# Optimization experiments

Measured on AMD Instinct MI355X. Metric: run time of the kernel, lower is better.

The kernel has to match this reference:

```python
import jax, jax.numpy as jnp
import numpy as np

G = 2048            # number of graphs in batch
NPG = 128           # nodes per graph (fixed, implied by Linear(128*hid, 1))
IN_C = 151
HID = 64
N = G * NPG
E = 2_097_152       # intra-graph edges, avg degree 8
NEG_SLOPE = 0.2


def setup_inputs() -> dict:
    key = jax.random.key(0)
    ks = jax.random.split(key, 8)
    x = jax.random.normal(ks[0], (N, IN_C), dtype=jnp.float32)
    # intra-graph random edges: pick a graph, then src/dst within it
    g = jax.random.randint(ks[1], (E,), 0, G)
    src = g * NPG + jax.random.randint(ks[2], (E,), 0, NPG)
    dst = g * NPG + jax.random.randint(ks[3], (E,), 0, NPG)
    edge_index = jnp.stack([src, dst]).astype(jnp.int32)   # [2, E]
    W1 = jax.random.normal(ks[4], (IN_C, HID), jnp.float32) / np.sqrt(IN_C)
    att_src = jax.random.normal(ks[5], (HID,), jnp.float32) * 0.1
    att_dst = jax.random.normal(ks[6], (HID,), jnp.float32) * 0.1
    b1 = jnp.zeros((HID,), jnp.float32)
    Wlin = jax.random.normal(ks[7], (NPG * HID, 1), jnp.float32) / np.sqrt(NPG * HID)
    blin = jnp.zeros((1,), jnp.float32)
    return {"x": x, "edge_index": edge_index, "W1": W1, "att_src": att_src,
            "att_dst": att_dst, "b1": b1, "Wlin": Wlin, "blin": blin}


def gat_conv(x, edge_index, W, a_src, a_dst, b):
    """PyG GATConv, heads=1, concat=True, add_self_loops=True."""
    n = x.shape[0]
    h = x @ W                                   # [N, HID] transformed features
    loops = jnp.arange(n, dtype=edge_index.dtype)
    src = jnp.concatenate([edge_index[0], loops])
    dst = jnp.concatenate([edge_index[1], loops])
    # edge score: a_src . h[j] + a_dst . h[i], j->i
    alpha = (h @ a_src)[src] + (h @ a_dst)[dst]            # [E+N]
    alpha = jax.nn.leaky_relu(alpha, NEG_SLOPE)
    # segment softmax over incoming edges of each target node
    amax = jax.ops.segment_max(alpha, dst, num_segments=n)
    ex = jnp.exp(alpha - amax[dst])
    denom = jax.ops.segment_sum(ex, dst, num_segments=n)
    w = ex / denom[dst]                                    # [E+N]
    out = jax.ops.segment_sum(h[src] * w[:, None], dst, num_segments=n)
    return out + b


def reference(x, edge_index, W1, att_src, att_dst, b1, Wlin, blin):
    h = jax.nn.relu(gat_conv(x, edge_index, W1, att_src, att_dst, b1))  # [N, HID]
    h = h.reshape(G, NPG * HID)        # linearize(x, batch): 128 nodes/graph
    logits = h @ Wlin + blin           # [G, 1]
    return jax.nn.sigmoid(logits)
```

## Files before the change

kernel.cpp:

```cpp
#include <hip/hip_runtime.h>
#include <hip/hip_bf16.h>

#define G_ 2048
#define NPG_ 128
#define INC_ 151
#define HID_ 64
#define NNODES_ (G_ * NPG_)
#define NEDGES_ 2097152

typedef __hip_bfloat16 bf16;
typedef short bf16x8v __attribute__((ext_vector_type(8)));
typedef float f32x4 __attribute__((ext_vector_type(4)));

static __device__ __forceinline__ short f2bs(float f) {
    __hip_bfloat16 b = __float2bfloat16(f);
    return __builtin_bit_cast(short, b);
}
static __device__ __forceinline__ float b2f(short s) {
    unsigned int u = ((unsigned int)(unsigned short)s) << 16;
    return __builtin_bit_cast(float, u);
}

__global__ void __launch_bounds__(256) k0_prep(const float* __restrict__ W1,
                                              bf16* __restrict__ Bt) {
    int i = blockIdx.x * 256 + threadIdx.x;
    if (i >= 64 * 168) return;
    int n = i / 168, k = i - n * 168;
    float v = (k < 151) ? W1[k * 64 + n] : 0.f;
    Bt[i] = __float2bfloat16(v);
}

__global__ void __launch_bounds__(256) k1_mfma(
        const float* __restrict__ x, const bf16* __restrict__ Bt,
        const float* __restrict__ att_src, const float* __restrict__ att_dst,
        bf16* __restrict__ h, float* __restrict__ as_, float* __restrict__ ad_) {
    __shared__ __align__(16) bf16 Bs[64 * 168];
    const int tid = threadIdx.x;
    const int rowbase = blockIdx.x * 64;

    {
        const uint4* s = (const uint4*)Bt;
        uint4* d = (uint4*)Bs;
        for (int i = tid; i < 1344; i += 256) d[i] = s[i];
    }
    __syncthreads();

    const int wv = tid >> 6, lane = tid & 63;
    const int quad = lane >> 4, m = lane & 15;
    const int row = rowbase + wv * 16 + m;
    const float* xr = x + (size_t)row * 151;

    f32x4 acc[4];
#pragma unroll
    for (int t = 0; t < 4; t++) acc[t] = (f32x4){0.f, 0.f, 0.f, 0.f};

#pragma unroll
    for (int ks = 0; ks < 5; ks++) {
        const int k0 = ks * 32 + quad * 8;
        float a[8];
        if (ks < 4) {
#pragma unroll
            for (int e = 0; e < 8; e++) a[e] = xr[k0 + e];
        } else {
#pragma unroll
            for (int e = 0; e < 8; e++) {
                int c = k0 + e;
                a[e] = (c < 151) ? xr[c] : 0.f;
            }
        }
        bf16x8v af = {f2bs(a[0]), f2bs(a[1]), f2bs(a[2]), f2bs(a[3]),
                      f2bs(a[4]), f2bs(a[5]), f2bs(a[6]), f2bs(a[7])};
#pragma unroll
        for (int t = 0; t < 4; t++) {
            bf16x8v bfr = *(const bf16x8v*)&Bs[(t * 16 + m) * 168 + k0];
            acc[t] = __builtin_amdgcn_mfma_f32_16x16x32_bf16(af, bfr, acc[t], 0, 0, 0);
        }
    }

    float as4[4], ad4[4];
#pragma unroll
    for (int t = 0; t < 4; t++) {
        as4[t] = att_src[t * 16 + m];
        ad4[t] = att_dst[t * 16 + m];
    }
#pragma unroll
    for (int r = 0; r < 4; r++) {
        float s = acc[0][r] * as4[0] + acc[1][r] * as4[1] +
                  acc[2][r] * as4[2] + acc[3][r] * as4[3];
        float d = acc[0][r] * ad4[0] + acc[1][r] * ad4[1] +
                  acc[2][r] * ad4[2] + acc[3][r] * ad4[3];
#pragma unroll
        for (int off = 1; off <= 8; off <<= 1) {
            s += __shfl_xor(s, off);
            d += __shfl_xor(d, off);
        }
        const int node = rowbase + wv * 16 + quad * 4 + r;
        if (m == 0) { as_[node] = s; ad_[node] = d; }
#pragma unroll
        for (int t = 0; t < 4; t++) {
            float val = acc[t][r];
            float oth = __shfl_xor(val, 1);
            if (!(lane & 1)) {
                unsigned short lo = (unsigned short)f2bs(val);
                unsigned short hi = (unsigned short)f2bs(oth);
                unsigned int u = ((unsigned int)hi << 16) | lo;
                *(unsigned int*)&h[(size_t)node * 64 + t * 16 + m] = u;
            }
        }
    }
}

__global__ void __launch_bounds__(256) kC1_hist(const int* __restrict__ ei,
                                                unsigned int* __restrict__ bccount) {
    __shared__ unsigned int hist[256];
    const int tid = threadIdx.x;
    hist[tid] = 0;
    __syncthreads();
    const int e0 = blockIdx.x * 8192;
    for (int e = e0 + tid; e < e0 + 8192; e += 256)
        atomicAdd(&hist[ei[e] >> 10], 1u);
    __syncthreads();
    bccount[blockIdx.x * 256 + tid] = hist[tid];
}

__global__ void __launch_bounds__(256) kC2_scan(unsigned int* __restrict__ bccount,
                                                unsigned int* __restrict__ cbase,
                                                unsigned int* __restrict__ base) {
    __shared__ unsigned int ssum[256];
    const int tid = threadIdx.x;
    unsigned int run = 0;
#pragma unroll 4
    for (int b = 0; b < 256; b++) {
        unsigned int* p = &bccount[b * 256 + tid];
        unsigned int c = *p;
        *p = run;
        run += c;
    }
    ssum[tid] = run;
    __syncthreads();
    unsigned int tot = run;
    for (int off = 1; off < 256; off <<= 1) {
        unsigned int t = (tid >= off) ? ssum[tid - off] : 0;
        __syncthreads();
        ssum[tid] += t;
        __syncthreads();
    }
    cbase[tid] = ssum[tid] - tot;
    if (tid == 255) {
        cbase[256] = ssum[255];
        base[G_] = NEDGES_;
    }
}

__global__ void __launch_bounds__(256) kC3_scatter(const int* __restrict__ ei,
                                                   const unsigned int* __restrict__ bccount,
                                                   const unsigned int* __restrict__ cbase,
                                                   unsigned int* __restrict__ rbuf) {
    __shared__ unsigned int cur[256];
    const int tid = threadIdx.x;
    cur[tid] = cbase[tid] + bccount[blockIdx.x * 256 + tid];
    __syncthreads();
    const int e0 = blockIdx.x * 8192;
    for (int e = e0 + tid; e < e0 + 8192; e += 256) {
        int s = ei[e];
        int d = ei[NEDGES_ + e];
        int bk = s >> 10;
        unsigned int pos = atomicAdd(&cur[bk], 1u);
        rbuf[pos] = (((unsigned int)s & 1023u) << 7) | ((unsigned int)d & 127u);
    }
}

__global__ void __launch_bounds__(256) kC4_fine(const unsigned int* __restrict__ rbuf,
                                                const unsigned int* __restrict__ cbase,
                                                unsigned int* __restrict__ base,
                                                unsigned short* __restrict__ eb) {
    __shared__ unsigned int lcnt[8];
    __shared__ unsigned int cur[8];
    const int tid = threadIdx.x;
    const int b = blockIdx.x;
    const unsigned int s0 = cbase[b], s1 = cbase[b + 1];
    if (tid < 8) lcnt[tid] = 0;
    __syncthreads();
    for (unsigned int i = s0 + tid; i < s1; i += 256)
        atomicAdd(&lcnt[(rbuf[i] >> 14) & 7], 1u);
    __syncthreads();
    if (tid == 0) {
        unsigned int r = 0;
#pragma unroll
        for (int j = 0; j < 8; j++) {
            base[b * 8 + j] = s0 + r;
            cur[j] = s0 + r;
            r += lcnt[j];
        }
    }
    __syncthreads();
    const int lane = tid & 63;
    for (unsigned int i = s0 + tid; i < s1; i += 256) {
        unsigned int rec = rbuf[i];
        int gl = (rec >> 14) & 7;
        unsigned long long act = __ballot(1);
        unsigned long long b0 = __ballot(gl & 1);
        unsigned long long b1 = __ballot(gl & 2);
        unsigned long long b2 = __ballot(gl & 4);
        unsigned long long m = ((gl & 1) ? b0 : ~b0) &
                               ((gl & 2) ? b1 : ~b1) &
                               ((gl & 4) ? b2 : ~b2) & act;
        int leader = __builtin_ctzll(m);
        int rank = __builtin_popcountll(m & ((1ull << lane) - 1ull));
        unsigned int bp = 0;
        if (lane == leader)
            bp = atomicAdd(&cur[gl], (unsigned int)__builtin_popcountll(m));
        bp = __shfl((int)bp, leader);
        eb[bp + rank] = (unsigned short)(rec & 0x3FFFu);
    }
}

__global__ void __launch_bounds__(256) k3_graph(
        const unsigned short* __restrict__ eb, const unsigned int* __restrict__ base,
        const bf16* __restrict__ h,
        const float* __restrict__ as_, const float* __restrict__ ad_,
        const float* __restrict__ b1, const float* __restrict__ Wlin,
        const float* __restrict__ blin, float* __restrict__ out) {
    __shared__ __align__(16) unsigned char lds[52736];
    short* Ab = (short*)lds;
    float* S = (float*)(lds + 34816);
    short* hT = (short*)(lds + 34816);
    unsigned short* ec = (unsigned short*)(lds + 30720);
    float* dinv = (float*)(lds + 52224);

    const int tid = threadIdx.x;
    const int g = blockIdx.x;
    const unsigned int gb = base[g], ge = base[g + 1];
    const float* asg = as_ + (g << 7);
    const float* adg = ad_ + (g << 7);
    const unsigned int* hgu = (const unsigned int*)(h + ((size_t)g << 13));

    const unsigned int cnt = ge - gb;
    const unsigned int ccnt = cnt > 2048u ? 2048u : cnt;
    for (unsigned int k = tid; k < ccnt; k += 256) ec[k] = eb[gb + k];
    __syncthreads();

#pragma unroll 1
    for (int p = 0; p < 4; p++) {
        for (int i = tid; i < 1024; i += 256)
            ((float4*)S)[i] = make_float4(0.f, 0.f, 0.f, 0.f);
        __syncthreads();
        if (tid < 32) {
            int node = 32 * p + tid;
            float a = asg[node] + adg[node];
            a = (a > 0.f) ? a : 0.2f * a;
            atomicAdd(&S[(tid << 7) + node], __expf(a));
        }
        for (unsigned int k = tid; k < ccnt; k += 256) {
            unsigned int v = ec[k];
            int sl = v >> 7, dl = v & 127;
            if ((dl >> 5) == p) {
                float a = asg[sl] + adg[dl];
                a = (a > 0.f) ? a : 0.2f * a;
                atomicAdd(&S[((dl & 31) << 7) + sl], __expf(a));
            }
        }
        for (unsigned int k = gb + ccnt + tid; k < ge; k += 256) {
            unsigned int v = eb[k];
            int sl = v >> 7, dl = v & 127;
            if ((dl >> 5) == p) {
                float a = asg[sl] + adg[dl];
                a = (a > 0.f) ? a : 0.2f * a;
                atomicAdd(&S[((dl & 31) << 7) + sl], __expf(a));
            }
        }
        __syncthreads();
        {
            const float4* rp = (const float4*)&S[((tid >> 3) << 7) + ((tid & 7) << 4)];
            float s = 0.f;
#pragma unroll
            for (int q = 0; q < 4; q++) {
                float4 v = rp[q];
                s += v.x + v.y + v.z + v.w;
            }
            s += __shfl_xor(s, 1);
            s += __shfl_xor(s, 2);
            s += __shfl_xor(s, 4);
            if ((tid & 7) == 0) dinv[32 * p + (tid >> 3)] = 1.f / s;
        }
        for (int c = tid; c < 512; c += 256) {
            int r = c >> 4;
            int col = (c & 15) << 3;
            float4 v0 = ((const float4*)S)[c * 2];
            float4 v1 = ((const float4*)S)[c * 2 + 1];
            bf16x8v pk = {f2bs(v0.x), f2bs(v0.y), f2bs(v0.z), f2bs(v0.w),
                          f2bs(v1.x), f2bs(v1.y), f2bs(v1.z), f2bs(v1.w)};
            *(bf16x8v*)&Ab[(32 * p + r) * 136 + col] = pk;
        }
        __syncthreads();
    }

    for (int idx = tid; idx < 4096; idx += 256) {
        unsigned int u = hgu[idx];
        int j = idx >> 5, f2 = idx & 31;
        hT[(2 * f2) * 136 + j] = (short)(u & 0xFFFF);
        hT[(2 * f2 + 1) * 136 + j] = (short)(u >> 16);
    }
    __syncthreads();

    const int w = tid >> 6, lane = tid & 63;
    const int quad = lane >> 4, m = lane & 15;
    const int i0 = w * 32;
    f32x4 acc[2][4];
#pragma unroll
    for (int mt = 0; mt < 2; mt++)
#pragma unroll
        for (int nt = 0; nt < 4; nt++) acc[mt][nt] = (f32x4){0.f, 0.f, 0.f, 0.f};

#pragma unroll
    for (int ks = 0; ks < 4; ks++) {
        const int k0 = ks * 32 + quad * 8;
        bf16x8v a0 = *(const bf16x8v*)&Ab[(i0 + m) * 136 + k0];
        bf16x8v a1 = *(const bf16x8v*)&Ab[(i0 + 16 + m) * 136 + k0];
#pragma unroll
        for (int nt = 0; nt < 4; nt++) {
            bf16x8v bfr = *(const bf16x8v*)&hT[(nt * 16 + m) * 136 + k0];
            acc[0][nt] = __builtin_amdgcn_mfma_f32_16x16x32_bf16(a0, bfr, acc[0][nt], 0, 0, 0);
            acc[1][nt] = __builtin_amdgcn_mfma_f32_16x16x32_bf16(a1, bfr, acc[1][nt], 0, 0, 0);
        }
    }

    float dv[2][4];
#pragma unroll
    for (int mt = 0; mt < 2; mt++)
#pragma unroll
        for (int r = 0; r < 4; r++)
            dv[mt][r] = dinv[i0 + mt * 16 + quad * 4 + r];

    float p = 0.f;
#pragma unroll
    for (int nt = 0; nt < 4; nt++) {
        float bb = b1[nt * 16 + m];
#pragma unroll
        for (int mt = 0; mt < 2; mt++) {
#pragma unroll
            for (int r = 0; r < 4; r++) {
                int il = i0 + mt * 16 + quad * 4 + r;
                float v = acc[mt][nt][r] * dv[mt][r] + bb;
                v = v > 0.f ? v : 0.f;
                p += v * Wlin[il * 64 + nt * 16 + m];
            }
        }
    }
#pragma unroll
    for (int off = 32; off; off >>= 1) p += __shfl_xor(p, off);

    __syncthreads();
    if (lane == 0) S[w] = p;
    __syncthreads();
    if (tid == 0) {
        float logit = S[0] + S[1] + S[2] + S[3] + blin[0];
        out[g] = 1.f / (1.f + __expf(-logit));
    }
}

extern "C" void kernel_launch(void* const* d_in, const int* in_sizes, int n_in,
                              void* d_out, int out_size, void* d_ws, size_t ws_size,
                              hipStream_t stream) {
    (void)in_sizes; (void)n_in; (void)out_size; (void)ws_size;
    const float* x       = (const float*)d_in[0];
    const int*   ei      = (const int*)d_in[1];
    const float* W1      = (const float*)d_in[2];
    const float* att_src = (const float*)d_in[3];
    const float* att_dst = (const float*)d_in[4];
    const float* b1      = (const float*)d_in[5];
    const float* Wlin    = (const float*)d_in[6];
    const float* blin    = (const float*)d_in[7];
    float* out = (float*)d_out;

    char* ws = (char*)d_ws;
    bf16*           h       = (bf16*)ws;
    float*          as_     = (float*)(ws + 33554432);
    float*          ad_     = (float*)(ws + 34603008);
    bf16*           Bt      = (bf16*)(ws + 35651584);
    unsigned int*   bccount = (unsigned int*)(ws + 35717120);
    unsigned int*   cbase   = (unsigned int*)(ws + 35979264);
    unsigned int*   base    = (unsigned int*)(ws + 35983360);
    unsigned int*   rbuf    = (unsigned int*)(ws + 35995648);
    unsigned short* eb      = (unsigned short*)(ws + 44384256);

    k0_prep<<<42, 256, 0, stream>>>(W1, Bt);
    k1_mfma<<<NNODES_ / 64, 256, 0, stream>>>(x, Bt, att_src, att_dst, h, as_, ad_);
    kC1_hist<<<256, 256, 0, stream>>>(ei, bccount);
    kC2_scan<<<1, 256, 0, stream>>>(bccount, cbase, base);
    kC3_scatter<<<256, 256, 0, stream>>>(ei, bccount, cbase, rbuf);
    kC4_fine<<<256, 256, 0, stream>>>(rbuf, cbase, base, eb);
    k3_graph<<<G_, 256, 0, stream>>>(eb, base, h, as_, ad_, b1, Wlin, blin, out);
}
```

Measured before the change: 389.5 us.

## Bucket edges by graph and destination quarter, parallelize scan, fuse prep with histogram

The fine sort now groups edges by graph and by the 32-node destination quarter, 32 keys per coarse bucket. Each pass of the graph kernel therefore reads only its own edges instead of filtering the whole edge list four times, and the LDS edge cache is removed. The serial single-block scan is split into a 256-block column scan plus a small totals scan. The W1 prep kernel is merged into the histogram launch, and the row-sum normalization is folded into the bf16 packing loop. The cost is a 5-bit ballot match instead of 3 bits in the fine sort, and one extra launch for the split scan.

```diff
diff --git a/kernel.cpp b/kernel.cpp
--- a/kernel.cpp
+++ b/kernel.cpp
@@ -21,13 +21,28 @@
     return __builtin_bit_cast(float, u);
 }
 
-__global__ void __launch_bounds__(256) k0_prep(const float* __restrict__ W1,
-                                              bf16* __restrict__ Bt) {
-    int i = blockIdx.x * 256 + threadIdx.x;
-    if (i >= 64 * 168) return;
-    int n = i / 168, k = i - n * 168;
-    float v = (k < 151) ? W1[k * 64 + n] : 0.f;
-    Bt[i] = __float2bfloat16(v);
+__global__ void __launch_bounds__(256) k0C1(const float* __restrict__ W1,
+                                            bf16* __restrict__ Bt,
+                                            const int* __restrict__ ei,
+                                            unsigned int* __restrict__ bccount) {
+    __shared__ unsigned int hist[256];
+    const int tid = threadIdx.x;
+    if (blockIdx.x >= 256) {
+        int i = (blockIdx.x - 256) * 256 + tid;
+        if (i < 64 * 168) {
+            int n = i / 168, k = i - n * 168;
+            float v = (k < 151) ? W1[k * 64 + n] : 0.f;
+            Bt[i] = __float2bfloat16(v);
+        }
+        return;
+    }
+    hist[tid] = 0;
+    __syncthreads();
+    const int e0 = blockIdx.x * 8192;
+    for (int e = e0 + tid; e < e0 + 8192; e += 256)
+        atomicAdd(&hist[ei[e] >> 10], 1u);
+    __syncthreads();
+    bccount[blockIdx.x * 256 + tid] = hist[tid];
 }
 
 __global__ void __launch_bounds__(256) k1_mfma(
@@ -110,45 +125,41 @@
     }
 }
 
-__global__ void __launch_bounds__(256) kC1_hist(const int* __restrict__ ei,
-                                                unsigned int* __restrict__ bccount) {
-    __shared__ unsigned int hist[256];
-    const int tid = threadIdx.x;
-    hist[tid] = 0;
-    __syncthreads();
-    const int e0 = blockIdx.x * 8192;
-    for (int e = e0 + tid; e < e0 + 8192; e += 256)
-        atomicAdd(&hist[ei[e] >> 10], 1u);
-    __syncthreads();
-    bccount[blockIdx.x * 256 + tid] = hist[tid];
-}
-
-__global__ void __launch_bounds__(256) kC2_scan(unsigned int* __restrict__ bccount,
-                                                unsigned int* __restrict__ cbase,
-                                                unsigned int* __restrict__ base) {
-    __shared__ unsigned int ssum[256];
-    const int tid = threadIdx.x;
-    unsigned int run = 0;
-#pragma unroll 4
-    for (int b = 0; b < 256; b++) {
-        unsigned int* p = &bccount[b * 256 + tid];
-        unsigned int c = *p;
-        *p = run;
-        run += c;
-    }
-    ssum[tid] = run;
-    __syncthreads();
-    unsigned int tot = run;
+__global__ void __launch_bounds__(256) kC2a(unsigned int* __restrict__ bccount,
+                                            unsigned int* __restrict__ totals) {
+    __shared__ unsigned int sc[256];
+    const int tid = threadIdx.x, bk = blockIdx.x;
+    unsigned int c = bccount[tid * 256 + bk];
+    sc[tid] = c;
+    __syncthreads();
     for (int off = 1; off < 256; off <<= 1) {
-        unsigned int t = (tid >= off) ? ssum[tid - off] : 0;
-        __syncthreads();
-        ssum[tid] += t;
-        __syncthreads();
-    }
-    cbase[tid] = ssum[tid] - tot;
+        unsigned int v = (tid >= off) ? sc[tid - off] : 0;
+        __syncthreads();
+        sc[tid] += v;
+        __syncthreads();
+    }
+    bccount[tid * 256 + bk] = sc[tid] - c;
+    if (tid == 255) totals[bk] = sc[255];
+}
+
+__global__ void __launch_bounds__(256) kC2b(const unsigned int* __restrict__ totals,
+                                            unsigned int* __restrict__ cbase,
+                                            unsigned int* __restrict__ base4) {
+    __shared__ unsigned int sc[256];
+    const int tid = threadIdx.x;
+    unsigned int c = totals[tid];
+    sc[tid] = c;
+    __syncthreads();
+    for (int off = 1; off < 256; off <<= 1) {
+        unsigned int v = (tid >= off) ? sc[tid - off] : 0;
+        __syncthreads();
+        sc[tid] += v;
+        __syncthreads();
+    }
+    cbase[tid] = sc[tid] - c;
     if (tid == 255) {
-        cbase[256] = ssum[255];
-        base[G_] = NEDGES_;
+        cbase[256] = sc[255];
+        base4[G_ * 4] = NEDGES_;
     }
 }
 
@@ -172,23 +183,26 @@
 
 __global__ void __launch_bounds__(256) kC4_fine(const unsigned int* __restrict__ rbuf,
                                                 const unsigned int* __restrict__ cbase,
-                                                unsigned int* __restrict__ base,
+                                                unsigned int* __restrict__ base4,
                                                 unsigned short* __restrict__ eb) {
-    __shared__ unsigned int lcnt[8];
-    __shared__ unsigned int cur[8];
+    __shared__ unsigned int lcnt[32];
+    __shared__ unsigned int cur[32];
     const int tid = threadIdx.x;
     const int b = blockIdx.x;
     const unsigned int s0 = cbase[b], s1 = cbase[b + 1];
-    if (tid < 8) lcnt[tid] = 0;
-    __syncthreads();
-    for (unsigned int i = s0 + tid; i < s1; i += 256)
-        atomicAdd(&lcnt[(rbuf[i] >> 14) & 7], 1u);
+    if (tid < 32) lcnt[tid] = 0;
+    __syncthreads();
+    for (unsigned int i = s0 + tid; i < s1; i += 256) {
+        unsigned int rec = rbuf[i];
+        int key = ((rec >> 12) & 0x1C) | ((rec >> 5) & 3);
+        atomicAdd(&lcnt[key], 1u);
+    }
     __syncthreads();
     if (tid == 0) {
         unsigned int r = 0;
 #pragma unroll
-        for (int j = 0; j < 8; j++) {
-            base[b * 8 + j] = s0 + r;
+        for (int j = 0; j < 32; j++) {
+            base4[b * 32 + j] = s0 + r;
             cur[j] = s0 + r;
             r += lcnt[j];
         }
@@ -197,26 +211,25 @@
     const int lane = tid & 63;
     for (unsigned int i = s0 + tid; i < s1; i += 256) {
         unsigned int rec = rbuf[i];
-        int gl = (rec >> 14) & 7;
-        unsigned long long act = __ballot(1);
-        unsigned long long b0 = __ballot(gl & 1);
-        unsigned long long b1 = __ballot(gl & 2);
-        unsigned long long b2 = __ballot(gl & 4);
-        unsigned long long m = ((gl & 1) ? b0 : ~b0) &
-                               ((gl & 2) ? b1 : ~b1) &
-                               ((gl & 4) ? b2 : ~b2) & act;
+        int key = ((rec >> 12) & 0x1C) | ((rec >> 5) & 3);
+        unsigned long long m = __ballot(1);
+#pragma unroll
+        for (int bit = 0; bit < 5; bit++) {
+            unsigned long long bb = __ballot((key >> bit) & 1);
+            m &= ((key >> bit) & 1) ? bb : ~bb;
+        }
         int leader = __builtin_ctzll(m);
         int rank = __builtin_popcountll(m & ((1ull << lane) - 1ull));
         unsigned int bp = 0;
         if (lane == leader)
-            bp = atomicAdd(&cur[gl], (unsigned int)__builtin_popcountll(m));
+            bp = atomicAdd(&cur[key], (unsigned int)__builtin_popcountll(m));
         bp = __shfl((int)bp, leader);
         eb[bp + rank] = (unsigned short)(rec & 0x3FFFu);
     }
 }
 
 __global__ void __launch_bounds__(256) k3_graph(
-        const unsigned short* __restrict__ eb, const unsigned int* __restrict__ base,
+        const unsigned short* __restrict__ eb, const unsigned int* __restrict__ base4,
         const bf16* __restrict__ h,
         const float* __restrict__ as_, const float* __restrict__ ad_,
         const float* __restrict__ b1, const float* __restrict__ Wlin,
@@ -225,20 +238,13 @@
     short* Ab = (short*)lds;
     float* S = (float*)(lds + 34816);
     short* hT = (short*)(lds + 34816);
-    unsigned short* ec = (unsigned short*)(lds + 30720);
     float* dinv = (float*)(lds + 52224);
 
     const int tid = threadIdx.x;
     const int g = blockIdx.x;
-    const unsigned int gb = base[g], ge = base[g + 1];
     const float* asg = as_ + (g << 7);
     const float* adg = ad_ + (g << 7);
     const unsigned int* hgu = (const unsigned int*)(h + ((size_t)g << 13));
-
-    const unsigned int cnt = ge - gb;
-    const unsigned int ccnt = cnt > 2048u ? 2048u : cnt;
-    for (unsigned int k = tid; k < ccnt; k += 256) ec[k] = eb[gb + k];
-    __syncthreads();
 
 #pragma unroll 1
     for (int p = 0; p < 4; p++) {
@@ -251,46 +257,37 @@
             a = (a > 0.f) ? a : 0.2f * a;
             atomicAdd(&S[(tid << 7) + node], __expf(a));
         }
-        for (unsigned int k = tid; k < ccnt; k += 256) {
-            unsigned int v = ec[k];
-            int sl = v >> 7, dl = v & 127;
-            if ((dl >> 5) == p) {
-                float a = asg[sl] + adg[dl];
-                a = (a > 0.f) ? a : 0.2f * a;
-                atomicAdd(&S[((dl & 31) << 7) + sl], __expf(a));
-            }
-        }
-        for (unsigned int k = gb + ccnt + tid; k < ge; k += 256) {
+        const unsigned int q0 = base4[(g << 2) + p];
+        const unsigned int q1 = base4[(g << 2) + p + 1];
+        for (unsigned int k = q0 + tid; k < q1; k += 256) {
             unsigned int v = eb[k];
             int sl = v >> 7, dl = v & 127;
-            if ((dl >> 5) == p) {
-                float a = asg[sl] + adg[dl];
-                a = (a > 0.f) ? a : 0.2f * a;
-                atomicAdd(&S[((dl & 31) << 7) + sl], __expf(a));
-            }
-        }
-        __syncthreads();
-        {
-            const float4* rp = (const float4*)&S[((tid >> 3) << 7) + ((tid & 7) << 4)];
-            float s = 0.f;
-#pragma unroll
-            for (int q = 0; q < 4; q++) {
-                float4 v = rp[q];
-                s += v.x + v.y + v.z + v.w;
-            }
-            s += __shfl_xor(s, 1);
-            s += __shfl_xor(s, 2);
-            s += __shfl_xor(s, 4);
-            if ((tid & 7) == 0) dinv[32 * p + (tid >> 3)] = 1.f / s;
-        }
-        for (int c = tid; c < 512; c += 256) {
+            float a = asg[sl] + adg[dl];
+            a = (a > 0.f) ? a : 0.2f * a;
+            atomicAdd(&S[((dl & 31) << 7) + sl], __expf(a));
+        }
+        __syncthreads();
+        float rs[2];
+#pragma unroll
+        for (int hf = 0; hf < 2; hf++) {
+            int c = tid + (hf << 8);
             int r = c >> 4;
             int col = (c & 15) << 3;
             float4 v0 = ((const float4*)S)[c * 2];
             float4 v1 = ((const float4*)S)[c * 2 + 1];
+            rs[hf] = v0.x + v0.y + v0.z + v0.w + v1.x + v1.y + v1.z + v1.w;
             bf16x8v pk = {f2bs(v0.x), f2bs(v0.y), f2bs(v0.z), f2bs(v0.w),
                           f2bs(v1.x), f2bs(v1.y), f2bs(v1.z), f2bs(v1.w)};
             *(bf16x8v*)&Ab[(32 * p + r) * 136 + col] = pk;
+        }
+#pragma unroll
+        for (int off = 1; off <= 8; off <<= 1) {
+            rs[0] += __shfl_xor(rs[0], off);
+            rs[1] += __shfl_xor(rs[1], off);
+        }
+        if ((tid & 15) == 0) {
+            dinv[32 * p + (tid >> 4)] = 1.f / rs[0];
+            dinv[32 * p + 16 + (tid >> 4)] = 1.f / rs[1];
         }
         __syncthreads();
     }
@@ -380,15 +377,16 @@
     bf16*           Bt      = (bf16*)(ws + 35651584);
     unsigned int*   bccount = (unsigned int*)(ws + 35717120);
     unsigned int*   cbase   = (unsigned int*)(ws + 35979264);
-    unsigned int*   base    = (unsigned int*)(ws + 35983360);
-    unsigned int*   rbuf    = (unsigned int*)(ws + 35995648);
-    unsigned short* eb      = (unsigned short*)(ws + 44384256);
-
-    k0_prep<<<42, 256, 0, stream>>>(W1, Bt);
+    unsigned int*   totals  = (unsigned int*)(ws + 35983360);
+    unsigned int*   base4   = (unsigned int*)(ws + 35987456);
+    unsigned int*   rbuf    = (unsigned int*)(ws + 36024320);
+    unsigned short* eb      = (unsigned short*)(ws + 44412928);
+
+    k0C1<<<298, 256, 0, stream>>>(W1, Bt, ei, bccount);
     k1_mfma<<<NNODES_ / 64, 256, 0, stream>>>(x, Bt, att_src, att_dst, h, as_, ad_);
-    kC1_hist<<<256, 256, 0, stream>>>(ei, bccount);
-    kC2_scan<<<1, 256, 0, stream>>>(bccount, cbase, base);
+    kC2a<<<256, 256, 0, stream>>>(bccount, totals);
+    kC2b<<<1, 256, 0, stream>>>(totals, cbase, base4);
     kC3_scatter<<<256, 256, 0, stream>>>(ei, bccount, cbase, rbuf);
-    kC4_fine<<<256, 256, 0, stream>>>(rbuf, cbase, base, eb);
-    k3_graph<<<G_, 256, 0, stream>>>(eb, base, h, as_, ad_, b1, Wlin, blin, out);
-}
+    kC4_fine<<<256, 256, 0, stream>>>(rbuf, cbase, base4, eb);
+    k3_graph<<<G_, 256, 0, stream>>>(eb, base4, h, as_, ad_, b1, Wlin, blin, out);
+}
```

After: 370.3 us. -4.9%, faster.
